# Kernel optimization log

Measured on AMD Instinct MI355X. Metric: run time of the kernel, lower is better.

Reference implementation:

```python
import jax, jax.numpy as jnp
import numpy as np

B, L, H, P, A, T = 64, 256, 1024, 64, 512, 8


def setup_inputs() -> dict:
    key = jax.random.key(0)
    ks = jax.random.split(key, 9)
    return {
        "word_hiddens": jax.random.normal(ks[0], (B, L, H), dtype=jnp.float32),
        "pos_e1_embeddings": jax.random.normal(ks[1], (B, L, P), dtype=jnp.float32),
        "pos_e2_embeddings": jax.random.normal(ks[2], (B, L, P), dtype=jnp.float32),
        "e1_end": jax.random.randint(ks[3], (B,), 0, L, dtype=jnp.int32),
        "e2_end": jax.random.randint(ks[4], (B,), 0, L, dtype=jnp.int32),
        "type_embeddings": jax.random.normal(ks[5], (T, H), dtype=jnp.float32) * 0.03,
        "W_pos": jax.random.normal(ks[6], (H + 2 * P, A), dtype=jnp.float32) * 0.03,
        "W_ent": jax.random.normal(ks[7], (4 * H, A), dtype=jnp.float32) * 0.02,
        "v": jax.random.normal(ks[8], (A,), dtype=jnp.float32) * 0.05,
    }


def _latent_type(e_h, type_emb):
    # alpha = softmax(e_h @ C^T); latent type = alpha @ C   (C: [T, latent])
    scores = jnp.einsum("bh,th->bt", e_h, type_emb)
    alpha = jax.nn.softmax(scores, axis=-1)
    return jnp.einsum("bt,th->bh", alpha, type_emb)


def reference(word_hiddens, pos_e1_embeddings, pos_e2_embeddings, e1_end, e2_end,
              type_embeddings, W_pos, W_ent, v):
    b, seq_len, h = word_hiddens.shape
    batch_idx = jnp.arange(b)
    e1_h = word_hiddens[batch_idx, e1_end]          # [B, H]
    e2_h = word_hiddens[batch_idx, e2_end]          # [B, H]
    e1_type = _latent_type(e1_h, type_embeddings)   # [B, H]
    e2_type = _latent_type(e2_h, type_embeddings)   # [B, H]

    entity_features = jnp.concatenate([e1_h, e1_type, e2_h, e2_type], axis=-1)  # [B, 4H]
    pos_features = jnp.concatenate([word_hiddens, pos_e1_embeddings, pos_e2_embeddings], axis=-1)  # [B, L, H+2P]

    dense_pos = jnp.einsum("blf,fa->bla", pos_features, W_pos)   # [B, L, A]
    dense_ent = entity_features @ W_ent                          # [B, A]
    # Faithful to original tf.repeat(axis=1)+reshape (element-interleaved, not a broadcast)
    dense_ent_r = jnp.repeat(dense_ent, seq_len, axis=1).reshape(b, seq_len, -1)  # [B, L, A]

    u = jnp.tanh(dense_pos + dense_ent_r)            # [B, L, A]
    vu = jnp.einsum("bla,a->bl", u, v)               # [B, L]
    alpha = jax.nn.softmax(vu, axis=-1)              # [B, L]
    z = jnp.einsum("blh,bl->bh", word_hiddens, alpha)  # [B, H]
    return z
```

## Files before the change

kernel.cpp:

```cpp
#include <hip/hip_runtime.h>
#include <hip/hip_bf16.h>
#include <math.h>

#define B_ 64
#define L_ 256
#define H_ 1024
#define P_ 64
#define A_ 512
#define T_ 8
#define KDIM 1152
#define NSTEP 36

typedef __attribute__((ext_vector_type(8))) __bf16 bf16x8;
typedef __attribute__((ext_vector_type(4))) float f32x4;

__device__ __forceinline__ float bf2f(ushort u) {
  union { unsigned int i; float f; } v; v.i = ((unsigned int)u) << 16; return v.f;
}
__device__ __forceinline__ ushort f2bf_rne(float f) {
  union { float f; unsigned int i; } v; v.f = f;
  unsigned int r = v.i + 0x7FFFu + ((v.i >> 16) & 1u);
  return (ushort)(r >> 16);
}
__device__ __forceinline__ unsigned int pack2_rne(float a, float b) {
  return (unsigned int)f2bf_rne(a) | ((unsigned int)f2bf_rne(b) << 16);
}

template <bool BF16>
__device__ __forceinline__ float ld1(const void* p, size_t i) {
  if (BF16) return bf2f(((const ushort*)p)[i]);
  return ((const float*)p)[i];
}
template <bool BF16>
__device__ __forceinline__ float4 ld4(const void* p, size_t i) {
  if (BF16) {
    ushort4 u = *(const ushort4*)((const ushort*)p + i);
    return (float4){bf2f(u.x), bf2f(u.y), bf2f(u.z), bf2f(u.w)};
  }
  return *(const float4*)((const float*)p + i);
}

template <bool BF16>
__global__ __launch_bounds__(256) void build_wts(const void* __restrict__ W,
                                                 ushort* __restrict__ WTs) {
  __shared__ ushort tile[32][33];
  const int s  = blockIdx.x >> 4;
  const int at = blockIdx.x & 15;
  const int tx = threadIdx.x & 31;
  const int ty = threadIdx.x >> 5;
#pragma unroll
  for (int i = 0; i < 4; ++i) {
    size_t idx = (size_t)(s * 32 + ty + i * 8) * A_ + at * 32 + tx;
    ushort u;
    if (BF16) u = ((const ushort*)W)[idx];
    else u = f2bf_rne(((const float*)W)[idx]);
    tile[ty + i * 8][tx] = u;
  }
  __syncthreads();
#pragma unroll
  for (int i = 0; i < 4; ++i) {
    WTs[(size_t)s * (A_ * 32) + (size_t)(at * 32 + ty + i * 8) * 32 + tx] =
        tile[tx][ty + i * 8];
  }
}

template <bool BF16>
__global__ __launch_bounds__(256) void entity_features_k(
    const void* __restrict__ wh, const int* __restrict__ e1e,
    const int* __restrict__ e2e, const void* __restrict__ temb,
    float* __restrict__ EF) {
  const int b = blockIdx.x;
  const int tid = threadIdx.x;
  __shared__ float eh1[1024];
  __shared__ float eh2[1024];
  __shared__ float part[256][16];
  __shared__ float scores[16];
  __shared__ float alpha[16];

  const size_t o1 = ((size_t)b * L_ + e1e[b]) * H_;
  const size_t o2 = ((size_t)b * L_ + e2e[b]) * H_;
  for (int h = tid; h < 1024; h += 256) {
    eh1[h] = ld1<BF16>(wh, o1 + h);
    eh2[h] = ld1<BF16>(wh, o2 + h);
  }
  __syncthreads();

  float p[16];
#pragma unroll
  for (int t = 0; t < 16; ++t) p[t] = 0.f;
  for (int h = tid; h < 1024; h += 256) {
    float a1 = eh1[h], a2 = eh2[h];
#pragma unroll
    for (int t = 0; t < 8; ++t) {
      float c = ld1<BF16>(temb, t * 1024 + h);
      p[t] += a1 * c;
      p[8 + t] += a2 * c;
    }
  }
#pragma unroll
  for (int t = 0; t < 16; ++t) part[tid][t] = p[t];
  __syncthreads();
  if (tid < 16) {
    float s = 0.f;
    for (int i = 0; i < 256; ++i) s += part[i][tid];
    scores[tid] = s;
  }
  __syncthreads();
  if (tid < 2) {
    const int base = tid * 8;
    float mx = scores[base];
    for (int t = 1; t < 8; ++t) mx = fmaxf(mx, scores[base + t]);
    float sum = 0.f;
    float e[8];
    for (int t = 0; t < 8; ++t) { e[t] = __expf(scores[base + t] - mx); sum += e[t]; }
    float inv = 1.f / sum;
    for (int t = 0; t < 8; ++t) alpha[base + t] = e[t] * inv;
  }
  __syncthreads();

  float* efb = EF + (size_t)b * 4096;
  for (int h = tid; h < 1024; h += 256) {
    float l1 = 0.f, l2 = 0.f;
#pragma unroll
    for (int t = 0; t < 8; ++t) {
      float c = ld1<BF16>(temb, t * 1024 + h);
      l1 += alpha[t] * c;
      l2 += alpha[8 + t] * c;
    }
    efb[h] = eh1[h];
    efb[1024 + h] = l1;
    efb[2048 + h] = eh2[h];
    efb[3072 + h] = l2;
  }
}

template <bool BF16>
__global__ __launch_bounds__(256) void ent_gemm(const float* __restrict__ EF,
                                                const void* __restrict__ went,
                                                float* __restrict__ part) {
  const int mh = blockIdx.x & 1;
  const int nb = (blockIdx.x >> 1) & 3;
  const int kb = blockIdx.x >> 3;
  const int tid = threadIdx.x;
  __shared__ float efs[32][128];

  const int k0 = kb * 128;
  {
    const int kq = (tid & 31) * 4;
    for (int m = tid >> 5; m < 32; m += 8) {
      *(float4*)&efs[m][kq] = *(const float4*)&EF[(size_t)(mh * 32 + m) * 4096 + k0 + kq];
    }
  }
  __syncthreads();

  const int n0 = nb * 128 + (tid & 31) * 4;
  const int mg = (tid >> 5) * 4;
  float acc[4][4];
#pragma unroll
  for (int i = 0; i < 4; ++i)
#pragma unroll
    for (int j = 0; j < 4; ++j) acc[i][j] = 0.f;

  for (int k = 0; k < 128; ++k) {
    float4 w = ld4<BF16>(went, (size_t)(k0 + k) * A_ + n0);
#pragma unroll
    for (int i = 0; i < 4; ++i) {
      float e = efs[mg + i][k];
      acc[i][0] += e * w.x;
      acc[i][1] += e * w.y;
      acc[i][2] += e * w.z;
      acc[i][3] += e * w.w;
    }
  }
#pragma unroll
  for (int i = 0; i < 4; ++i) {
    *(float4*)&part[((size_t)kb * 64 + mh * 32 + mg + i) * A_ + n0] =
        (float4){acc[i][0], acc[i][1], acc[i][2], acc[i][3]};
  }
}

__global__ __launch_bounds__(256) void ent_reduce(const float* __restrict__ part,
                                                  float* __restrict__ dense_ent) {
  const int idx = blockIdx.x * 256 + threadIdx.x;
  float s = 0.f;
#pragma unroll
  for (int kb = 0; kb < 32; ++kb) s += part[(size_t)kb * 32768 + idx];
  dense_ent[idx] = s;
}

template <bool BF16>
__global__ __launch_bounds__(256) void fused_gemm_vu(
    const void* __restrict__ wh, const void* __restrict__ pe1,
    const void* __restrict__ pe2, const ushort* __restrict__ WTs,
    const float* __restrict__ dense_ent, const void* __restrict__ vvec,
    float* __restrict__ vu_part) {
  __shared__ __align__(16) ushort Abuf[2][64 * 40];
  __shared__ __align__(16) ushort Bbuf[2][128 * 40];
  __shared__ float vu_s[4][64];

  const int tid = threadIdx.x;
  const int nb = blockIdx.x & 3;
  const int mb = blockIdx.x >> 2;
  const int rbase = mb * 64;
  const int wave = tid >> 6;
  const int lane = tid & 63;
  const int quad = lane >> 4;
  const int col = lane & 15;
  const int wr = wave >> 1;
  const int wc = wave & 1;

  const int arow = tid >> 2;
  const int akq = (tid & 3) * 8;
  const int myrow = rbase + arow;
  const int brow = tid >> 1;
  const int bk0 = (tid & 1) * 16;
  const ushort* bbase = WTs + (size_t)(nb * 128 + brow) * 32 + bk0;

  f32x4 acc[2][4];
#pragma unroll
  for (int i = 0; i < 2; ++i)
#pragma unroll
    for (int j = 0; j < 4; ++j) acc[i][j] = (f32x4){0.f, 0.f, 0.f, 0.f};

  uint4 aR, bR0, bR1;

  {
    const size_t off = (size_t)myrow * H_ + akq;
    if (BF16) {
      aR = *(const uint4*)((const ushort*)wh + off);
    } else {
      float4 f0 = *(const float4*)((const float*)wh + off);
      float4 f1 = *(const float4*)((const float*)wh + off + 4);
      aR.x = pack2_rne(f0.x, f0.y); aR.y = pack2_rne(f0.z, f0.w);
      aR.z = pack2_rne(f1.x, f1.y); aR.w = pack2_rne(f1.z, f1.w);
    }
    bR0 = *(const uint4*)(bbase + 0);
    bR1 = *(const uint4*)(bbase + 8);
  }
  {
    *(uint4*)&Abuf[0][arow * 40 + akq] = aR;
    ushort* bd = &Bbuf[0][brow * 40 + bk0];
    *(uint4*)(bd + 0) = bR0;
    *(uint4*)(bd + 8) = bR1;
  }
  __syncthreads();

  for (int s = 0; s < NSTEP; ++s) {
    const int cur = s & 1;

    if (s < NSTEP - 1) {
      const int sn = s + 1;
      const void* srcA;
      int ldA, k0A;
      if (sn < 32)      { srcA = wh;  ldA = H_; k0A = sn * 32; }
      else if (sn < 34) { srcA = pe1; ldA = P_; k0A = (sn - 32) * 32; }
      else              { srcA = pe2; ldA = P_; k0A = (sn - 34) * 32; }
      const size_t off = (size_t)myrow * ldA + k0A + akq;
      if (BF16) {
        aR = *(const uint4*)((const ushort*)srcA + off);
      } else {
        float4 f0 = *(const float4*)((const float*)srcA + off);
        float4 f1 = *(const float4*)((const float*)srcA + off + 4);
        aR.x = pack2_rne(f0.x, f0.y); aR.y = pack2_rne(f0.z, f0.w);
        aR.z = pack2_rne(f1.x, f1.y); aR.w = pack2_rne(f1.z, f1.w);
      }
      const ushort* bs = bbase + (size_t)sn * (A_ * 32);
      bR0 = *(const uint4*)(bs + 0);
      bR1 = *(const uint4*)(bs + 8);
    }

    bf16x8 af[2], bfr[4];
#pragma unroll
    for (int mf = 0; mf < 2; ++mf)
      af[mf] = *(const bf16x8*)&Abuf[cur][(wr * 32 + mf * 16 + col) * 40 + quad * 8];
#pragma unroll
    for (int nf = 0; nf < 4; ++nf)
      bfr[nf] = *(const bf16x8*)&Bbuf[cur][(wc * 64 + nf * 16 + col) * 40 + quad * 8];
#pragma unroll
    for (int mf = 0; mf < 2; ++mf)
#pragma unroll
      for (int nf = 0; nf < 4; ++nf)
        acc[mf][nf] = __builtin_amdgcn_mfma_f32_16x16x32_bf16(af[mf], bfr[nf], acc[mf][nf], 0, 0, 0);

    if (s < NSTEP - 1) {
      const int nxt = cur ^ 1;
      *(uint4*)&Abuf[nxt][arow * 40 + akq] = aR;
      ushort* bd = &Bbuf[nxt][brow * 40 + bk0];
      *(uint4*)(bd + 0) = bR0;
      *(uint4*)(bd + 8) = bR1;
      __syncthreads();
    }
  }

  float vv[4];
#pragma unroll
  for (int nf = 0; nf < 4; ++nf)
    vv[nf] = ld1<BF16>(vvec, nb * 128 + wc * 64 + nf * 16 + col);

#pragma unroll
  for (int mf = 0; mf < 2; ++mf) {
    const int row0 = wr * 32 + mf * 16 + quad * 4;
    const int r0 = rbase + row0;
    const int bidx = r0 >> 8;
    const int l0 = r0 & 255;
    const float* ebase = dense_ent + bidx * A_ + 2 * l0 + (nb >> 1);
    float e0 = ebase[0], e1 = ebase[2], e2 = ebase[4], e3 = ebase[6];
    float s0 = 0.f, s1 = 0.f, s2 = 0.f, s3 = 0.f;
#pragma unroll
    for (int nf = 0; nf < 4; ++nf) {
      float vn = vv[nf];
      s0 += tanhf(acc[mf][nf][0] + e0) * vn;
      s1 += tanhf(acc[mf][nf][1] + e1) * vn;
      s2 += tanhf(acc[mf][nf][2] + e2) * vn;
      s3 += tanhf(acc[mf][nf][3] + e3) * vn;
    }
    s0 += __shfl_xor(s0, 1); s0 += __shfl_xor(s0, 2); s0 += __shfl_xor(s0, 4); s0 += __shfl_xor(s0, 8);
    s1 += __shfl_xor(s1, 1); s1 += __shfl_xor(s1, 2); s1 += __shfl_xor(s1, 4); s1 += __shfl_xor(s1, 8);
    s2 += __shfl_xor(s2, 1); s2 += __shfl_xor(s2, 2); s2 += __shfl_xor(s2, 4); s2 += __shfl_xor(s2, 8);
    s3 += __shfl_xor(s3, 1); s3 += __shfl_xor(s3, 2); s3 += __shfl_xor(s3, 4); s3 += __shfl_xor(s3, 8);
    if (col == 0) {
      vu_s[wave][row0 + 0] = s0;
      vu_s[wave][row0 + 1] = s1;
      vu_s[wave][row0 + 2] = s2;
      vu_s[wave][row0 + 3] = s3;
    }
  }
  __syncthreads();
  if (tid < 64) {
    const int wrr = tid >> 5;
    float s = vu_s[wrr * 2][tid] + vu_s[wrr * 2 + 1][tid];
    vu_part[(size_t)nb * (B_ * L_) + rbase + tid] = s;
  }
}

template <bool BF16>
__global__ __launch_bounds__(256) void softmax_z(const void* __restrict__ wh,
                                                 const float* __restrict__ vu_part,
                                                 void* __restrict__ out) {
  const int b = blockIdx.x >> 2;
  const int hq = blockIdx.x & 3;
  const int tid = threadIdx.x;
  __shared__ float alpha[256];
  __shared__ float red[256];

  float x = 0.f;
#pragma unroll
  for (int p = 0; p < 4; ++p) x += vu_part[(size_t)p * (B_ * L_) + b * L_ + tid];
  red[tid] = x;
  __syncthreads();
  for (int s = 128; s > 0; s >>= 1) {
    if (tid < s) red[tid] = fmaxf(red[tid], red[tid + s]);
    __syncthreads();
  }
  float m = red[0];
  __syncthreads();
  float e = __expf(x - m);
  red[tid] = e;
  __syncthreads();
  for (int s = 128; s > 0; s >>= 1) {
    if (tid < s) red[tid] += red[tid + s];
    __syncthreads();
  }
  alpha[tid] = e / red[0];
  __syncthreads();

  const int h = hq * 256 + tid;
  const size_t base = (size_t)b * L_ * H_ + h;
  float a0 = 0.f, a1 = 0.f, a2 = 0.f, a3 = 0.f;
  float a4 = 0.f, a5 = 0.f, a6 = 0.f, a7 = 0.f;
  for (int l = 0; l < 256; l += 8) {
    a0 += alpha[l + 0] * ld1<BF16>(wh, base + (size_t)(l + 0) * H_);
    a1 += alpha[l + 1] * ld1<BF16>(wh, base + (size_t)(l + 1) * H_);
    a2 += alpha[l + 2] * ld1<BF16>(wh, base + (size_t)(l + 2) * H_);
    a3 += alpha[l + 3] * ld1<BF16>(wh, base + (size_t)(l + 3) * H_);
    a4 += alpha[l + 4] * ld1<BF16>(wh, base + (size_t)(l + 4) * H_);
    a5 += alpha[l + 5] * ld1<BF16>(wh, base + (size_t)(l + 5) * H_);
    a6 += alpha[l + 6] * ld1<BF16>(wh, base + (size_t)(l + 6) * H_);
    a7 += alpha[l + 7] * ld1<BF16>(wh, base + (size_t)(l + 7) * H_);
  }
  float z = ((a0 + a1) + (a2 + a3)) + ((a4 + a5) + (a6 + a7));
  if (BF16) ((ushort*)out)[b * H_ + h] = f2bf_rne(z);
  else ((float*)out)[b * H_ + h] = z;
}

extern "C" void kernel_launch(void* const* d_in, const int* in_sizes, int n_in,
                              void* d_out, int out_size, void* d_ws, size_t ws_size,
                              hipStream_t stream) {
  const void* wh   = d_in[0];
  const void* pe1  = d_in[1];
  const void* pe2  = d_in[2];
  const int*  e1e  = (const int*)d_in[3];
  const int*  e2e  = (const int*)d_in[4];
  const void* temb = d_in[5];
  const void* wpos = d_in[6];
  const void* went = d_in[7];
  const void* vvec = d_in[8];

  const bool bf16 = (in_sizes[0] == (int)(B_ * L_ * H_ * 2));

  char* ws = (char*)d_ws;
  ushort* WTs      = (ushort*)ws;
  float* dense_ent = (float*)(ws + 1179648);
  float* vu_part   = (float*)(ws + 1310720);
  float* EF        = (float*)(ws + 1310720);
  float* part      = (float*)(ws + 2359296);

  if (bf16) {
    build_wts<true ><<<dim3(576),  dim3(256), 0, stream>>>(wpos, WTs);
    entity_features_k<true ><<<dim3(64), dim3(256), 0, stream>>>(wh, e1e, e2e, temb, EF);
    ent_gemm<true ><<<dim3(256),  dim3(256), 0, stream>>>(EF, went, part);
    ent_reduce<<<dim3(128), dim3(256), 0, stream>>>(part, dense_ent);
    fused_gemm_vu<true ><<<dim3(1024), dim3(256), 0, stream>>>(wh, pe1, pe2, WTs, dense_ent, vvec, vu_part);
    softmax_z<true ><<<dim3(256), dim3(256), 0, stream>>>(wh, vu_part, d_out);
  } else {
    build_wts<false><<<dim3(576),  dim3(256), 0, stream>>>(wpos, WTs);
    entity_features_k<false><<<dim3(64), dim3(256), 0, stream>>>(wh, e1e, e2e, temb, EF);
    ent_gemm<false><<<dim3(256),  dim3(256), 0, stream>>>(EF, went, part);
    ent_reduce<<<dim3(128), dim3(256), 0, stream>>>(part, dense_ent);
    fused_gemm_vu<false><<<dim3(1024), dim3(256), 0, stream>>>(wh, pe1, pe2, WTs, dense_ent, vvec, vu_part);
    softmax_z<false><<<dim3(256), dim3(256), 0, stream>>>(wh, vu_part, d_out);
  }
}
```

Before: 192.9 us.

## Enlarge GEMM tile to 128 rows, swizzle LDS, deepen prefetch, merge prep kernels

The main fused GEMM+tanh+v kernel now computes 128x128 tiles instead of 64x128. It uses XOR-swizzled unpadded LDS layouts, a two-register-set prefetch pipeline that keeps two K-steps of global loads in flight, and a block-index remap so blocks sharing a row tile run close together. The goal is less redundant loading of activations and weights, better latency hiding and fewer bank conflicts, at the cost of higher register pressure and fewer blocks (512). The weight-transpose and entity-feature kernels are merged into one launch to cut a kernel launch, and the entity GEMM inner loop gets an unroll pragma.

```diff
diff --git a/kernel.cpp b/kernel.cpp
--- a/kernel.cpp
+++ b/kernel.cpp
@@ -8,7 +8,6 @@
 #define P_ 64
 #define A_ 512
 #define T_ 8
-#define KDIM 1152
 #define NSTEP 36
 
 typedef __attribute__((ext_vector_type(8))) __bf16 bf16x8;
@@ -41,96 +40,95 @@
 }
 
 template <bool BF16>
-__global__ __launch_bounds__(256) void build_wts(const void* __restrict__ W,
-                                                 ushort* __restrict__ WTs) {
-  __shared__ ushort tile[32][33];
-  const int s  = blockIdx.x >> 4;
-  const int at = blockIdx.x & 15;
-  const int tx = threadIdx.x & 31;
-  const int ty = threadIdx.x >> 5;
-#pragma unroll
-  for (int i = 0; i < 4; ++i) {
-    size_t idx = (size_t)(s * 32 + ty + i * 8) * A_ + at * 32 + tx;
-    ushort u;
-    if (BF16) u = ((const ushort*)W)[idx];
-    else u = f2bf_rne(((const float*)W)[idx]);
-    tile[ty + i * 8][tx] = u;
-  }
-  __syncthreads();
-#pragma unroll
-  for (int i = 0; i < 4; ++i) {
-    WTs[(size_t)s * (A_ * 32) + (size_t)(at * 32 + ty + i * 8) * 32 + tx] =
-        tile[tx][ty + i * 8];
-  }
-}
-
-template <bool BF16>
-__global__ __launch_bounds__(256) void entity_features_k(
+__global__ __launch_bounds__(256) void prep_k(
+    const void* __restrict__ wpos, ushort* __restrict__ WTs,
     const void* __restrict__ wh, const int* __restrict__ e1e,
     const int* __restrict__ e2e, const void* __restrict__ temb,
     float* __restrict__ EF) {
-  const int b = blockIdx.x;
-  const int tid = threadIdx.x;
-  __shared__ float eh1[1024];
-  __shared__ float eh2[1024];
-  __shared__ float part[256][16];
-  __shared__ float scores[16];
-  __shared__ float alpha[16];
-
-  const size_t o1 = ((size_t)b * L_ + e1e[b]) * H_;
-  const size_t o2 = ((size_t)b * L_ + e2e[b]) * H_;
-  for (int h = tid; h < 1024; h += 256) {
-    eh1[h] = ld1<BF16>(wh, o1 + h);
-    eh2[h] = ld1<BF16>(wh, o2 + h);
-  }
-  __syncthreads();
-
-  float p[16];
-#pragma unroll
-  for (int t = 0; t < 16; ++t) p[t] = 0.f;
-  for (int h = tid; h < 1024; h += 256) {
-    float a1 = eh1[h], a2 = eh2[h];
-#pragma unroll
-    for (int t = 0; t < 8; ++t) {
-      float c = ld1<BF16>(temb, t * 1024 + h);
-      p[t] += a1 * c;
-      p[8 + t] += a2 * c;
-    }
-  }
-#pragma unroll
-  for (int t = 0; t < 16; ++t) part[tid][t] = p[t];
-  __syncthreads();
-  if (tid < 16) {
-    float s = 0.f;
-    for (int i = 0; i < 256; ++i) s += part[i][tid];
-    scores[tid] = s;
-  }
-  __syncthreads();
-  if (tid < 2) {
-    const int base = tid * 8;
-    float mx = scores[base];
-    for (int t = 1; t < 8; ++t) mx = fmaxf(mx, scores[base + t]);
-    float sum = 0.f;
-    float e[8];
-    for (int t = 0; t < 8; ++t) { e[t] = __expf(scores[base + t] - mx); sum += e[t]; }
-    float inv = 1.f / sum;
-    for (int t = 0; t < 8; ++t) alpha[base + t] = e[t] * inv;
-  }
-  __syncthreads();
-
-  float* efb = EF + (size_t)b * 4096;
-  for (int h = tid; h < 1024; h += 256) {
-    float l1 = 0.f, l2 = 0.f;
-#pragma unroll
-    for (int t = 0; t < 8; ++t) {
-      float c = ld1<BF16>(temb, t * 1024 + h);
-      l1 += alpha[t] * c;
-      l2 += alpha[8 + t] * c;
-    }
-    efb[h] = eh1[h];
-    efb[1024 + h] = l1;
-    efb[2048 + h] = eh2[h];
-    efb[3072 + h] = l2;
+  if (blockIdx.x < 576) {
+    __shared__ ushort tile[32][33];
+    const int s  = blockIdx.x >> 4;
+    const int at = blockIdx.x & 15;
+    const int tx = threadIdx.x & 31;
+    const int ty = threadIdx.x >> 5;
+#pragma unroll
+    for (int i = 0; i < 4; ++i) {
+      size_t idx = (size_t)(s * 32 + ty + i * 8) * A_ + at * 32 + tx;
+      ushort u;
+      if (BF16) u = ((const ushort*)wpos)[idx];
+      else u = f2bf_rne(((const float*)wpos)[idx]);
+      tile[ty + i * 8][tx] = u;
+    }
+    __syncthreads();
+#pragma unroll
+    for (int i = 0; i < 4; ++i) {
+      WTs[(size_t)s * (A_ * 32) + (size_t)(at * 32 + ty + i * 8) * 32 + tx] =
+          tile[tx][ty + i * 8];
+    }
+  } else {
+    const int b = blockIdx.x - 576;
+    const int tid = threadIdx.x;
+    __shared__ float eh1[1024];
+    __shared__ float eh2[1024];
+    __shared__ float part[256][16];
+    __shared__ float scores[16];
+    __shared__ float alpha[16];
+
+    const size_t o1 = ((size_t)b * L_ + e1e[b]) * H_;
+    const size_t o2 = ((size_t)b * L_ + e2e[b]) * H_;
+    for (int h = tid; h < 1024; h += 256) {
+      eh1[h] = ld1<BF16>(wh, o1 + h);
+      eh2[h] = ld1<BF16>(wh, o2 + h);
+    }
+    __syncthreads();
+
+    float p[16];
+#pragma unroll
+    for (int t = 0; t < 16; ++t) p[t] = 0.f;
+    for (int h = tid; h < 1024; h += 256) {
+      float a1 = eh1[h], a2 = eh2[h];
+#pragma unroll
+      for (int t = 0; t < 8; ++t) {
+        float c = ld1<BF16>(temb, t * 1024 + h);
+        p[t] += a1 * c;
+        p[8 + t] += a2 * c;
+      }
+    }
+#pragma unroll
+    for (int t = 0; t < 16; ++t) part[tid][t] = p[t];
+    __syncthreads();
+    if (tid < 16) {
+      float s = 0.f;
+      for (int i = 0; i < 256; ++i) s += part[i][tid];
+      scores[tid] = s;
+    }
+    __syncthreads();
+    if (tid < 2) {
+      const int base = tid * 8;
+      float mx = scores[base];
+      for (int t = 1; t < 8; ++t) mx = fmaxf(mx, scores[base + t]);
+      float sum = 0.f;
+      float e[8];
+      for (int t = 0; t < 8; ++t) { e[t] = __expf(scores[base + t] - mx); sum += e[t]; }
+      float inv = 1.f / sum;
+      for (int t = 0; t < 8; ++t) alpha[base + t] = e[t] * inv;
+    }
+    __syncthreads();
+
+    float* efb = EF + (size_t)b * 4096;
+    for (int h = tid; h < 1024; h += 256) {
+      float l1 = 0.f, l2 = 0.f;
+#pragma unroll
+      for (int t = 0; t < 8; ++t) {
+        float c = ld1<BF16>(temb, t * 1024 + h);
+        l1 += alpha[t] * c;
+        l2 += alpha[8 + t] * c;
+      }
+      efb[h] = eh1[h];
+      efb[1024 + h] = l1;
+      efb[2048 + h] = eh2[h];
+      efb[3072 + h] = l2;
+    }
   }
 }
 
@@ -161,6 +159,7 @@
 #pragma unroll
     for (int j = 0; j < 4; ++j) acc[i][j] = 0.f;
 
+#pragma unroll 4
   for (int k = 0; k < 128; ++k) {
     float4 w = ld4<BF16>(went, (size_t)(k0 + k) * A_ + n0);
 #pragma unroll
@@ -189,19 +188,21 @@
 }
 
 template <bool BF16>
-__global__ __launch_bounds__(256) void fused_gemm_vu(
+__global__ __launch_bounds__(256, 2) void fused_gemm_vu(
     const void* __restrict__ wh, const void* __restrict__ pe1,
     const void* __restrict__ pe2, const ushort* __restrict__ WTs,
     const float* __restrict__ dense_ent, const void* __restrict__ vvec,
     float* __restrict__ vu_part) {
-  __shared__ __align__(16) ushort Abuf[2][64 * 40];
-  __shared__ __align__(16) ushort Bbuf[2][128 * 40];
-  __shared__ float vu_s[4][64];
+  __shared__ __align__(16) ushort Abuf[2][128 * 32];
+  __shared__ __align__(16) ushort Bbuf[2][128 * 32];
+  __shared__ float vu_s[4][128];
 
   const int tid = threadIdx.x;
-  const int nb = blockIdx.x & 3;
-  const int mb = blockIdx.x >> 2;
-  const int rbase = mb * 64;
+  const int pid = blockIdx.x;
+  const int wid = (pid & 7) * 64 + (pid >> 3);
+  const int nb = wid & 3;
+  const int mb = wid >> 2;
+  const int rbase = mb * 128;
   const int wave = tid >> 6;
   const int lane = tid & 63;
   const int quad = lane >> 4;
@@ -209,85 +210,134 @@
   const int wr = wave >> 1;
   const int wc = wave & 1;
 
-  const int arow = tid >> 2;
-  const int akq = (tid & 3) * 8;
-  const int myrow = rbase + arow;
+  int aoff[4], boff[4];
+#pragma unroll
+  for (int mf = 0; mf < 4; ++mf) {
+    const int ra = wr * 64 + mf * 16 + col;
+    aoff[mf] = ra * 32 + ((quad ^ ((ra >> 1) & 3)) << 3);
+    const int rb = wc * 64 + mf * 16 + col;
+    boff[mf] = rb * 32 + ((quad ^ ((rb >> 1) & 3)) << 3);
+  }
+
   const int brow = tid >> 1;
-  const int bk0 = (tid & 1) * 16;
-  const ushort* bbase = WTs + (size_t)(nb * 128 + brow) * 32 + bk0;
-
-  f32x4 acc[2][4];
-#pragma unroll
-  for (int i = 0; i < 2; ++i)
+  const int bc0 = (tid & 1) * 2;
+  const int sB0 = brow * 32 + ((bc0 ^ ((brow >> 1) & 3)) << 3);
+  const size_t bsrc_off = (size_t)(nb * 128 + brow) * 32 + (size_t)(tid & 1) * 16;
+
+  const int ar0 = tid >> 2, aq = tid & 3;
+  const int ar1 = 64 + ar0;
+  const int sA0 = ar0 * 32 + ((aq ^ ((ar0 >> 1) & 3)) << 3);
+  const int sA1 = ar1 * 32 + ((aq ^ ((ar1 >> 1) & 3)) << 3);
+
+  f32x4 acc[4][4];
+#pragma unroll
+  for (int i = 0; i < 4; ++i)
 #pragma unroll
     for (int j = 0; j < 4; ++j) acc[i][j] = (f32x4){0.f, 0.f, 0.f, 0.f};
 
-  uint4 aR, bR0, bR1;
-
-  {
-    const size_t off = (size_t)myrow * H_ + akq;
+  float4 fX0a, fX0b, fX1a, fX1b; uint4 uX0, uX1; uint4 bX0, bX1;
+  float4 fY0a, fY0b, fY1a, fY1b; uint4 uY0, uY1; uint4 bY0, bY1;
+
+  auto ISSUE_X = [&](int s) {
+    const void* src; int ld, k0;
+    if (s < 32)      { src = wh;  ld = H_; k0 = s * 32; }
+    else if (s < 34) { src = pe1; ld = P_; k0 = (s - 32) * 32; }
+    else             { src = pe2; ld = P_; k0 = (s - 34) * 32; }
     if (BF16) {
-      aR = *(const uint4*)((const ushort*)wh + off);
+      const ushort* p = (const ushort*)src + (size_t)(rbase + brow) * ld + k0 + (tid & 1) * 16;
+      uX0 = *(const uint4*)p;
+      uX1 = *(const uint4*)(p + 8);
     } else {
-      float4 f0 = *(const float4*)((const float*)wh + off);
-      float4 f1 = *(const float4*)((const float*)wh + off + 4);
-      aR.x = pack2_rne(f0.x, f0.y); aR.y = pack2_rne(f0.z, f0.w);
-      aR.z = pack2_rne(f1.x, f1.y); aR.w = pack2_rne(f1.z, f1.w);
-    }
-    bR0 = *(const uint4*)(bbase + 0);
-    bR1 = *(const uint4*)(bbase + 8);
-  }
-  {
-    *(uint4*)&Abuf[0][arow * 40 + akq] = aR;
-    ushort* bd = &Bbuf[0][brow * 40 + bk0];
-    *(uint4*)(bd + 0) = bR0;
-    *(uint4*)(bd + 8) = bR1;
-  }
-  __syncthreads();
-
-  for (int s = 0; s < NSTEP; ++s) {
-    const int cur = s & 1;
-
-    if (s < NSTEP - 1) {
-      const int sn = s + 1;
-      const void* srcA;
-      int ldA, k0A;
-      if (sn < 32)      { srcA = wh;  ldA = H_; k0A = sn * 32; }
-      else if (sn < 34) { srcA = pe1; ldA = P_; k0A = (sn - 32) * 32; }
-      else              { srcA = pe2; ldA = P_; k0A = (sn - 34) * 32; }
-      const size_t off = (size_t)myrow * ldA + k0A + akq;
-      if (BF16) {
-        aR = *(const uint4*)((const ushort*)srcA + off);
-      } else {
-        float4 f0 = *(const float4*)((const float*)srcA + off);
-        float4 f1 = *(const float4*)((const float*)srcA + off + 4);
-        aR.x = pack2_rne(f0.x, f0.y); aR.y = pack2_rne(f0.z, f0.w);
-        aR.z = pack2_rne(f1.x, f1.y); aR.w = pack2_rne(f1.z, f1.w);
-      }
-      const ushort* bs = bbase + (size_t)sn * (A_ * 32);
-      bR0 = *(const uint4*)(bs + 0);
-      bR1 = *(const uint4*)(bs + 8);
-    }
-
-    bf16x8 af[2], bfr[4];
-#pragma unroll
-    for (int mf = 0; mf < 2; ++mf)
-      af[mf] = *(const bf16x8*)&Abuf[cur][(wr * 32 + mf * 16 + col) * 40 + quad * 8];
-#pragma unroll
-    for (int nf = 0; nf < 4; ++nf)
-      bfr[nf] = *(const bf16x8*)&Bbuf[cur][(wc * 64 + nf * 16 + col) * 40 + quad * 8];
-#pragma unroll
-    for (int mf = 0; mf < 2; ++mf)
+      const float* p0 = (const float*)src + (size_t)(rbase + ar0) * ld + k0 + aq * 8;
+      fX0a = *(const float4*)p0;
+      fX0b = *(const float4*)(p0 + 4);
+      const float* p1 = (const float*)src + (size_t)(rbase + ar1) * ld + k0 + aq * 8;
+      fX1a = *(const float4*)p1;
+      fX1b = *(const float4*)(p1 + 4);
+    }
+    const ushort* bs = WTs + (size_t)s * (A_ * 32) + bsrc_off;
+    bX0 = *(const uint4*)bs;
+    bX1 = *(const uint4*)(bs + 8);
+  };
+  auto ISSUE_Y = [&](int s) {
+    const void* src; int ld, k0;
+    if (s < 32)      { src = wh;  ld = H_; k0 = s * 32; }
+    else if (s < 34) { src = pe1; ld = P_; k0 = (s - 32) * 32; }
+    else             { src = pe2; ld = P_; k0 = (s - 34) * 32; }
+    if (BF16) {
+      const ushort* p = (const ushort*)src + (size_t)(rbase + brow) * ld + k0 + (tid & 1) * 16;
+      uY0 = *(const uint4*)p;
+      uY1 = *(const uint4*)(p + 8);
+    } else {
+      const float* p0 = (const float*)src + (size_t)(rbase + ar0) * ld + k0 + aq * 8;
+      fY0a = *(const float4*)p0;
+      fY0b = *(const float4*)(p0 + 4);
+      const float* p1 = (const float*)src + (size_t)(rbase + ar1) * ld + k0 + aq * 8;
+      fY1a = *(const float4*)p1;
+      fY1b = *(const float4*)(p1 + 4);
+    }
+    const ushort* bs = WTs + (size_t)s * (A_ * 32) + bsrc_off;
+    bY0 = *(const uint4*)bs;
+    bY1 = *(const uint4*)(bs + 8);
+  };
+  auto STORE_X = [&](int buf) {
+    if (BF16) {
+      *(uint4*)&Abuf[buf][sB0] = uX0;
+      *(uint4*)&Abuf[buf][sB0 ^ 8] = uX1;
+    } else {
+      uint4 u0 = {pack2_rne(fX0a.x, fX0a.y), pack2_rne(fX0a.z, fX0a.w),
+                  pack2_rne(fX0b.x, fX0b.y), pack2_rne(fX0b.z, fX0b.w)};
+      *(uint4*)&Abuf[buf][sA0] = u0;
+      uint4 u1 = {pack2_rne(fX1a.x, fX1a.y), pack2_rne(fX1a.z, fX1a.w),
+                  pack2_rne(fX1b.x, fX1b.y), pack2_rne(fX1b.z, fX1b.w)};
+      *(uint4*)&Abuf[buf][sA1] = u1;
+    }
+    *(uint4*)&Bbuf[buf][sB0] = bX0;
+    *(uint4*)&Bbuf[buf][sB0 ^ 8] = bX1;
+  };
+  auto STORE_Y = [&](int buf) {
+    if (BF16) {
+      *(uint4*)&Abuf[buf][sB0] = uY0;
+      *(uint4*)&Abuf[buf][sB0 ^ 8] = uY1;
+    } else {
+      uint4 u0 = {pack2_rne(fY0a.x, fY0a.y), pack2_rne(fY0a.z, fY0a.w),
+                  pack2_rne(fY0b.x, fY0b.y), pack2_rne(fY0b.z, fY0b.w)};
+      *(uint4*)&Abuf[buf][sA0] = u0;
+      uint4 u1 = {pack2_rne(fY1a.x, fY1a.y), pack2_rne(fY1a.z, fY1a.w),
+                  pack2_rne(fY1b.x, fY1b.y), pack2_rne(fY1b.z, fY1b.w)};
+      *(uint4*)&Abuf[buf][sA1] = u1;
+    }
+    *(uint4*)&Bbuf[buf][sB0] = bY0;
+    *(uint4*)&Bbuf[buf][sB0 ^ 8] = bY1;
+  };
+  auto COMPUTE = [&](int buf) {
+    bf16x8 af[4], bfr[4];
+#pragma unroll
+    for (int mf = 0; mf < 4; ++mf) af[mf] = *(const bf16x8*)&Abuf[buf][aoff[mf]];
+#pragma unroll
+    for (int nf = 0; nf < 4; ++nf) bfr[nf] = *(const bf16x8*)&Bbuf[buf][boff[nf]];
+#pragma unroll
+    for (int mf = 0; mf < 4; ++mf)
 #pragma unroll
       for (int nf = 0; nf < 4; ++nf)
-        acc[mf][nf] = __builtin_amdgcn_mfma_f32_16x16x32_bf16(af[mf], bfr[nf], acc[mf][nf], 0, 0, 0);
-
-    if (s < NSTEP - 1) {
-      const int nxt = cur ^ 1;
-      *(uint4*)&Abuf[nxt][arow * 40 + akq] = aR;
-      ushort* bd = &Bbuf[nxt][brow * 40 + bk0];
-      *(uint4*)(bd + 0) = bR0;
-      *(uint4*)(bd + 8) = bR1;
+        acc[mf][nf] =
+            __builtin_amdgcn_mfma_f32_16x16x32_bf16(af[mf], bfr[nf], acc[mf][nf], 0, 0, 0);
+  };
+
+  ISSUE_X(0);
+  ISSUE_Y(1);
+  STORE_X(0);
+  __syncthreads();
+
+  for (int s = 0; s < NSTEP; s += 2) {
+    if (s + 2 < NSTEP) ISSUE_X(s + 2);
+    COMPUTE(0);
+    STORE_Y(1);
+    __syncthreads();
+    if (s + 3 < NSTEP) ISSUE_Y(s + 3);
+    COMPUTE(1);
+    if (s + 2 < NSTEP) {
+      STORE_X(0);
       __syncthreads();
     }
   }
@@ -298,8 +348,8 @@
     vv[nf] = ld1<BF16>(vvec, nb * 128 + wc * 64 + nf * 16 + col);
 
 #pragma unroll
-  for (int mf = 0; mf < 2; ++mf) {
-    const int row0 = wr * 32 + mf * 16 + quad * 4;
+  for (int mf = 0; mf < 4; ++mf) {
+    const int row0 = wr * 64 + mf * 16 + quad * 4;
     const int r0 = rbase + row0;
     const int bidx = r0 >> 8;
     const int l0 = r0 & 255;
@@ -326,8 +376,8 @@
     }
   }
   __syncthreads();
-  if (tid < 64) {
-    const int wrr = tid >> 5;
+  if (tid < 128) {
+    const int wrr = tid >> 6;
     float s = vu_s[wrr * 2][tid] + vu_s[wrr * 2 + 1][tid];
     vu_part[(size_t)nb * (B_ * L_) + rbase + tid] = s;
   }
@@ -406,18 +456,16 @@
   float* part      = (float*)(ws + 2359296);
 
   if (bf16) {
-    build_wts<true ><<<dim3(576),  dim3(256), 0, stream>>>(wpos, WTs);
-    entity_features_k<true ><<<dim3(64), dim3(256), 0, stream>>>(wh, e1e, e2e, temb, EF);
-    ent_gemm<true ><<<dim3(256),  dim3(256), 0, stream>>>(EF, went, part);
+    prep_k<true ><<<dim3(640), dim3(256), 0, stream>>>(wpos, WTs, wh, e1e, e2e, temb, EF);
+    ent_gemm<true ><<<dim3(256), dim3(256), 0, stream>>>(EF, went, part);
     ent_reduce<<<dim3(128), dim3(256), 0, stream>>>(part, dense_ent);
-    fused_gemm_vu<true ><<<dim3(1024), dim3(256), 0, stream>>>(wh, pe1, pe2, WTs, dense_ent, vvec, vu_part);
+    fused_gemm_vu<true ><<<dim3(512), dim3(256), 0, stream>>>(wh, pe1, pe2, WTs, dense_ent, vvec, vu_part);
     softmax_z<true ><<<dim3(256), dim3(256), 0, stream>>>(wh, vu_part, d_out);
   } else {
-    build_wts<false><<<dim3(576),  dim3(256), 0, stream>>>(wpos, WTs);
-    entity_features_k<false><<<dim3(64), dim3(256), 0, stream>>>(wh, e1e, e2e, temb, EF);
-    ent_gemm<false><<<dim3(256),  dim3(256), 0, stream>>>(EF, went, part);
+    prep_k<false><<<dim3(640), dim3(256), 0, stream>>>(wpos, WTs, wh, e1e, e2e, temb, EF);
+    ent_gemm<false><<<dim3(256), dim3(256), 0, stream>>>(EF, went, part);
     ent_reduce<<<dim3(128), dim3(256), 0, stream>>>(part, dense_ent);
-    fused_gemm_vu<false><<<dim3(1024), dim3(256), 0, stream>>>(wh, pe1, pe2, WTs, dense_ent, vvec, vu_part);
+    fused_gemm_vu<false><<<dim3(512), dim3(256), 0, stream>>>(wh, pe1, pe2, WTs, dense_ent, vvec, vu_part);
     softmax_z<false><<<dim3(256), dim3(256), 0, stream>>>(wh, vu_part, d_out);
   }
 }
```

Result: no change. 193.3 us (+0.2%).
